# Kernel tuning notes

Measured on AMD Instinct MI355X. Metric: run time of the kernel, lower is better.

## Reference

```python
import jax, jax.numpy as jnp
import numpy as np
import math

EPS = 1e-12  # F.normalize default eps

def _l2_normalize(x):
    n = jnp.sqrt(jnp.sum(x * x, axis=-1, keepdims=True))
    return x / jnp.maximum(n, EPS)

def setup_inputs() -> dict:
    key = jax.random.key(0)
    k1, k2 = jax.random.split(key)
    B, F, C = 16384, 1024, 1000
    features = jax.random.normal(k1, (B, F), dtype=jnp.float32)
    prototypes = jax.random.normal(k2, (C, F), dtype=jnp.float32)
    distance_scale = jnp.ones((1,), dtype=jnp.float32)
    temperature = jnp.ones((1,), dtype=jnp.float32)
    return {"features": features, "prototypes": prototypes,
            "distance_scale": distance_scale, "temperature": temperature}

def reference(features, prototypes, distance_scale, temperature):
    # L2-normalize both sides (F.normalize, p=2, eps=1e-12)
    f = _l2_normalize(features)      # [B, F]
    p = _l2_normalize(prototypes)    # [C, F]
    # Pairwise Euclidean distance. For unit vectors ||f-p||^2 = 2 - 2 f.p,
    # clamped at 0 for numerical safety; then / sqrt(2).
    sim = jnp.einsum('bf,cf->bc', f, p)                  # [B, C]
    sq = jnp.maximum(2.0 - 2.0 * sim, 0.0)
    distances = jnp.sqrt(sq) / jnp.float32(math.sqrt(2.0))
    iso = jnp.abs(distance_scale) * distances            # [B, C]
    logits = -(iso + jnp.mean(iso, axis=1, keepdims=True))
    return logits / temperature
```

## Files before the change

### kernel.cpp

```cpp
#include <hip/hip_runtime.h>
#include <hip/hip_bf16.h>
#include <math.h>

#define B_ROWS 16384
#define C_COLS 1000
#define C_PAD  1024
#define FDIM   1024
#define FBLKS  4096
#define FP8_SCALE 256.0f
#define INV_SIM   (1.0f / (FP8_SCALE * FP8_SCALE))

typedef __attribute__((ext_vector_type(8))) short bf16x8;
typedef __attribute__((ext_vector_type(4))) float f32x4;
typedef __attribute__((ext_vector_type(4))) int   i32x4;
typedef __attribute__((ext_vector_type(8))) int   i32x8;

#define GLD_LDS(gp, lp) __builtin_amdgcn_global_load_lds( \
    (__attribute__((address_space(1))) void*)(gp),        \
    (__attribute__((address_space(3))) void*)(lp), 16, 0, 0)

__global__ __launch_bounds__(256) void normalize_all(
    const float* __restrict__ feat, const float* __restrict__ prot,
    unsigned char* __restrict__ fb, unsigned char* __restrict__ pb,
    float* __restrict__ rowsum)
{
    const int lane = threadIdx.x & 63;
    const int wave = threadIdx.x >> 6;

    if (blockIdx.x < 64) rowsum[blockIdx.x * 256 + threadIdx.x] = 0.0f;

    const float* in;
    unsigned char* out;
    int row, nvalid;
    if (blockIdx.x < FBLKS) {
        row = blockIdx.x * 4 + wave;  in = feat; out = fb; nvalid = B_ROWS;
    } else {
        row = (blockIdx.x - FBLKS) * 4 + wave;  in = prot; out = pb; nvalid = C_COLS;
    }
    unsigned char* orow = out + (size_t)row * FDIM;

    if (row >= nvalid) {
        i32x4 z = {0, 0, 0, 0};
        ((i32x4*)orow)[lane] = z;
        return;
    }

    const float4* rp = (const float4*)(in + (size_t)row * FDIM);
    float4 v[4];
    float ss = 0.0f;
    #pragma unroll
    for (int c = 0; c < 4; ++c) {
        v[c] = rp[lane * 4 + c];
        ss += v[c].x * v[c].x + v[c].y * v[c].y + v[c].z * v[c].z + v[c].w * v[c].w;
    }
    #pragma unroll
    for (int off = 1; off < 64; off <<= 1) ss += __shfl_xor(ss, off, 64);
    const float inv = FP8_SCALE / sqrtf(fmaxf(ss, 1e-24f));

    i32x4 pk;
    #pragma unroll
    for (int c = 0; c < 4; ++c) {
        int w0 = __builtin_amdgcn_cvt_pk_fp8_f32(v[c].x * inv, v[c].y * inv, 0, false);
        w0     = __builtin_amdgcn_cvt_pk_fp8_f32(v[c].z * inv, v[c].w * inv, w0, true);
        pk[c] = w0;
    }
    ((i32x4*)orow)[lane] = pk;
}

__global__ __launch_bounds__(256) void gemm_dist(
    const unsigned char* __restrict__ A,
    const unsigned char* __restrict__ Bp,
    __hip_bfloat16* __restrict__ D,
    float* __restrict__ rowsum)
{
    __shared__ unsigned char As[128 * 128];
    __shared__ unsigned char Bs[128 * 128];

    const int tid  = threadIdx.x;
    const int lane = tid & 63;
    const int wave = tid >> 6;

    const int id  = blockIdx.x;
    const int xcd = id & 7;
    const int seq = id >> 3;
    const int bn  = seq & 7;
    const int bm  = xcd * 16 + (seq >> 3);

    const int waveM = (wave >> 1) * 64;
    const int waveN = (wave & 1) * 64;

    f32x4 acc[4][4] = {};

    const int srow8 = lane >> 3;
    const int sg    = (lane & 7) ^ srow8;
    const unsigned char* Abase = A  + ((size_t)(bm * 128 + wave * 8 + srow8)) * FDIM + sg * 16;
    const unsigned char* Bbase = Bp + ((size_t)(bn * 128 + wave * 8 + srow8)) * FDIM + sg * 16;

    const int q2   = (lane >> 4) * 2;
    const int bxor = lane & 7;
    const int fA = (waveM + (lane & 15)) * 128;
    const int fB = (waveN + (lane & 15)) * 128;
    const int pg0 = ((q2)     ^ bxor) * 16;
    const int pg1 = ((q2 + 1) ^ bxor) * 16;

    #pragma unroll 1
    for (int k0 = 0; k0 < FDIM; k0 += 128) {
        __syncthreads();
        #pragma unroll
        for (int r = 0; r < 4; ++r) {
            GLD_LDS(Abase + (size_t)(r * 32) * FDIM + k0, &As[(r * 32 + wave * 8) * 128]);
            GLD_LDS(Bbase + (size_t)(r * 32) * FDIM + k0, &Bs[(r * 32 + wave * 8) * 128]);
        }
        __syncthreads();

        i32x8 b[4];
        #pragma unroll
        for (int nt = 0; nt < 4; ++nt) {
            const i32x4 lo = *(const i32x4*)&Bs[fB + nt * 2048 + pg0];
            const i32x4 hi = *(const i32x4*)&Bs[fB + nt * 2048 + pg1];
            b[nt] = (i32x8){lo.x, lo.y, lo.z, lo.w, hi.x, hi.y, hi.z, hi.w};
        }
        #pragma unroll
        for (int mt = 0; mt < 4; ++mt) {
            const i32x4 lo = *(const i32x4*)&As[fA + mt * 2048 + pg0];
            const i32x4 hi = *(const i32x4*)&As[fA + mt * 2048 + pg1];
            const i32x8 a = (i32x8){lo.x, lo.y, lo.z, lo.w, hi.x, hi.y, hi.z, hi.w};
            #pragma unroll
            for (int nt = 0; nt < 4; ++nt)
                acc[mt][nt] = __builtin_amdgcn_mfma_scale_f32_16x16x128_f8f6f4(
                    a, b[nt], acc[mt][nt], 0, 0, 0, 127, 0, 127);
        }
    }

    const int row0 = bm * 128 + waveM;
    const int col0 = bn * 128 + waveN;
    #pragma unroll
    for (int mt = 0; mt < 4; ++mt) {
        #pragma unroll
        for (int r = 0; r < 4; ++r) {
            const int row = row0 + mt * 16 + (lane >> 4) * 4 + r;
            float part = 0.0f;
            #pragma unroll
            for (int nt = 0; nt < 4; ++nt) {
                const int col = col0 + nt * 16 + (lane & 15);
                const float sim = acc[mt][nt][r] * INV_SIM;
                const float dv = sqrtf(fmaxf(1.0f - sim, 0.0f));
                if (col < C_COLS) {
                    D[(size_t)row * C_COLS + col] = __float2bfloat16(dv);
                    part += dv;
                }
            }
            part += __shfl_xor(part, 1, 64);
            part += __shfl_xor(part, 2, 64);
            part += __shfl_xor(part, 4, 64);
            part += __shfl_xor(part, 8, 64);
            if ((lane & 15) == 0) atomicAdd(&rowsum[row], part);
        }
    }
}

__global__ __launch_bounds__(256) void finalize(
    const __hip_bfloat16* __restrict__ D, const float* __restrict__ rowsum,
    const float* __restrict__ scale, const float* __restrict__ temp,
    float* __restrict__ out)
{
    const size_t i = (size_t)blockIdx.x * 256 + threadIdx.x;
    const float a = -fabsf(scale[0]) / temp[0];
    const int row = (int)((i * 8) / C_COLS);
    const float m = rowsum[row] * (1.0f / (float)C_COLS);

    const bf16x8 dv = *(const bf16x8*)(D + i * 8);
    const __hip_bfloat16* dp = (const __hip_bfloat16*)&dv;
    float4 o0, o1;
    o0.x = a * (__bfloat162float(dp[0]) + m);
    o0.y = a * (__bfloat162float(dp[1]) + m);
    o0.z = a * (__bfloat162float(dp[2]) + m);
    o0.w = a * (__bfloat162float(dp[3]) + m);
    o1.x = a * (__bfloat162float(dp[4]) + m);
    o1.y = a * (__bfloat162float(dp[5]) + m);
    o1.z = a * (__bfloat162float(dp[6]) + m);
    o1.w = a * (__bfloat162float(dp[7]) + m);
    ((float4*)out)[i * 2]     = o0;
    ((float4*)out)[i * 2 + 1] = o1;
}

extern "C" void kernel_launch(void* const* d_in, const int* in_sizes, int n_in,
                              void* d_out, int out_size, void* d_ws, size_t ws_size,
                              hipStream_t stream)
{
    const float* features = (const float*)d_in[0];
    const float* protos   = (const float*)d_in[1];
    const float* dscale   = (const float*)d_in[2];
    const float* temp     = (const float*)d_in[3];
    float* out = (float*)d_out;

    char* ws = (char*)d_ws;
    unsigned char* fb = (unsigned char*)ws;
    unsigned char* pb = (unsigned char*)(ws + 16777216);
    __hip_bfloat16* D = (__hip_bfloat16*)(ws + 17825792);
    float* rowsum     = (float*)(ws + 50593792);

    normalize_all<<<FBLKS + C_PAD / 4, 256, 0, stream>>>(features, protos, fb, pb, rowsum);

    gemm_dist<<<1024, 256, 0, stream>>>(fb, pb, D, rowsum);

    finalize<<<(B_ROWS * C_COLS / 8) / 256, 256, 0, stream>>>(D, rowsum, dscale, temp, out);
}
```

Baseline: 159.3 us.

## Fuse distance GEMM and finalize via cooperative grid sync, keeping distances in registers

Adds a cooperative-launch kernel that computes the FP8 GEMM and distance values, accumulates per-row sums atomically, then waits on a grid-wide barrier. After the barrier it reads the completed row means and writes the final fp32 logits directly from registers. This removes the bf16 intermediate distance buffer (write and re-read of about 32 MB) and the separate finalize launch. In exchange, all 1024 blocks must be co-resident (launch bounds 256,4), which may limit registers, and the grid barrier adds sync cost. If cooperative launch is unavailable it falls back to the old two-kernel path.

```diff
diff --git a/kernel.cpp b/kernel.cpp
--- a/kernel.cpp
+++ b/kernel.cpp
@@ -1,4 +1,5 @@
 #include <hip/hip_runtime.h>
+#include <hip/hip_cooperative_groups.h>
 #include <hip/hip_bf16.h>
 #include <math.h>
 
@@ -65,6 +66,117 @@
         pk[c] = w0;
     }
     ((i32x4*)orow)[lane] = pk;
+}
+
+__global__ __launch_bounds__(256, 4) void gemm_dist_out(
+    const unsigned char* __restrict__ A,
+    const unsigned char* __restrict__ Bp,
+    float* __restrict__ rowsum,
+    const float* __restrict__ scale,
+    const float* __restrict__ temp,
+    float* __restrict__ out)
+{
+    __shared__ unsigned char As[128 * 128];
+    __shared__ unsigned char Bs[128 * 128];
+
+    const int tid  = threadIdx.x;
+    const int lane = tid & 63;
+    const int wave = tid >> 6;
+
+    const int id  = blockIdx.x;
+    const int xcd = id & 7;
+    const int seq = id >> 3;
+    const int bn  = seq & 7;
+    const int bm  = xcd * 16 + (seq >> 3);
+
+    const int waveM = (wave >> 1) * 64;
+    const int waveN = (wave & 1) * 64;
+
+    f32x4 acc[4][4] = {};
+
+    const int srow8 = lane >> 3;
+    const int sg    = (lane & 7) ^ srow8;
+    const unsigned char* Abase = A  + ((size_t)(bm * 128 + wave * 8 + srow8)) * FDIM + sg * 16;
+    const unsigned char* Bbase = Bp + ((size_t)(bn * 128 + wave * 8 + srow8)) * FDIM + sg * 16;
+
+    const int q2   = (lane >> 4) * 2;
+    const int bxor = lane & 7;
+    const int fA = (waveM + (lane & 15)) * 128;
+    const int fB = (waveN + (lane & 15)) * 128;
+    const int pg0 = ((q2)     ^ bxor) * 16;
+    const int pg1 = ((q2 + 1) ^ bxor) * 16;
+
+    #pragma unroll 1
+    for (int k0 = 0; k0 < FDIM; k0 += 128) {
+        __syncthreads();
+        #pragma unroll
+        for (int r = 0; r < 4; ++r) {
+            GLD_LDS(Abase + (size_t)(r * 32) * FDIM + k0, &As[(r * 32 + wave * 8) * 128]);
+            GLD_LDS(Bbase + (size_t)(r * 32) * FDIM + k0, &Bs[(r * 32 + wave * 8) * 128]);
+        }
+        __syncthreads();
+
+        i32x8 b[4];
+        #pragma unroll
+        for (int nt = 0; nt < 4; ++nt) {
+            const i32x4 lo = *(const i32x4*)&Bs[fB + nt * 2048 + pg0];
+            const i32x4 hi = *(const i32x4*)&Bs[fB + nt * 2048 + pg1];
+            b[nt] = (i32x8){lo.x, lo.y, lo.z, lo.w, hi.x, hi.y, hi.z, hi.w};
+        }
+        #pragma unroll
+        for (int mt = 0; mt < 4; ++mt) {
+            const i32x4 lo = *(const i32x4*)&As[fA + mt * 2048 + pg0];
+            const i32x4 hi = *(const i32x4*)&As[fA + mt * 2048 + pg1];
+            const i32x8 a = (i32x8){lo.x, lo.y, lo.z, lo.w, hi.x, hi.y, hi.z, hi.w};
+            #pragma unroll
+            for (int nt = 0; nt < 4; ++nt)
+                acc[mt][nt] = __builtin_amdgcn_mfma_scale_f32_16x16x128_f8f6f4(
+                    a, b[nt], acc[mt][nt], 0, 0, 0, 127, 0, 127);
+        }
+    }
+
+    const int row0 = bm * 128 + waveM;
+    const int col0 = bn * 128 + waveN;
+    #pragma unroll
+    for (int mt = 0; mt < 4; ++mt) {
+        #pragma unroll
+        for (int r = 0; r < 4; ++r) {
+            float part = 0.0f;
+            #pragma unroll
+            for (int nt = 0; nt < 4; ++nt) {
+                const float sim = acc[mt][nt][r] * INV_SIM;
+                const float dv = sqrtf(fmaxf(1.0f - sim, 0.0f));
+                acc[mt][nt][r] = dv;
+                const int col = col0 + nt * 16 + (lane & 15);
+                if (col < C_COLS) part += dv;
+            }
+            part += __shfl_xor(part, 1, 64);
+            part += __shfl_xor(part, 2, 64);
+            part += __shfl_xor(part, 4, 64);
+            part += __shfl_xor(part, 8, 64);
+            if ((lane & 15) == 0)
+                atomicAdd(&rowsum[row0 + mt * 16 + (lane >> 4) * 4 + r], part);
+        }
+    }
+
+    cooperative_groups::this_grid().sync();
+
+    const float aS = -fabsf(scale[0]) / temp[0];
+    #pragma unroll
+    for (int mt = 0; mt < 4; ++mt) {
+        #pragma unroll
+        for (int r = 0; r < 4; ++r) {
+            const int row = row0 + mt * 16 + (lane >> 4) * 4 + r;
+            const float m = __hip_atomic_load(&rowsum[row], __ATOMIC_RELAXED,
+                                              __HIP_MEMORY_SCOPE_AGENT) * (1.0f / (float)C_COLS);
+            #pragma unroll
+            for (int nt = 0; nt < 4; ++nt) {
+                const int col = col0 + nt * 16 + (lane & 15);
+                if (col < C_COLS)
+                    out[(size_t)row * C_COLS + col] = aS * (acc[mt][nt][r] + m);
+            }
+        }
+    }
 }
 
 __global__ __launch_bounds__(256) void gemm_dist(
@@ -202,7 +314,37 @@
 
     normalize_all<<<FBLKS + C_PAD / 4, 256, 0, stream>>>(features, protos, fb, pb, rowsum);
 
-    gemm_dist<<<1024, 256, 0, stream>>>(fb, pb, D, rowsum);
-
-    finalize<<<(B_ROWS * C_COLS / 8) / 256, 256, 0, stream>>>(D, rowsum, dscale, temp, out);
-}
+    static int use_coop = -1;
+    if (use_coop < 0) {
+        int dev = 0;
+        (void)hipGetDevice(&dev);
+        int coopOK = 0;
+        (void)hipDeviceGetAttribute(&coopOK, hipDeviceAttributeCooperativeLaunch, dev);
+        int numCU = 0;
+        (void)hipDeviceGetAttribute(&numCU, hipDeviceAttributeMultiprocessorCount, dev);
+        int maxB = 0;
+        hipError_t oe = hipOccupancyMaxActiveBlocksPerMultiprocessor(
+            &maxB, reinterpret_cast<const void*>(gemm_dist_out), 256, 0);
+        use_coop = (coopOK && oe == hipSuccess && numCU > 0 &&
+                    (long)maxB * numCU >= 1024) ? 1 : 0;
+    }
+
+    if (use_coop) {
+        const unsigned char* gA = fb;
+        const unsigned char* gB = pb;
+        float* gR = rowsum;
+        const float* gS = dscale;
+        const float* gT = temp;
+        float* gO = out;
+        void* kargs[] = { (void*)&gA, (void*)&gB, (void*)&gR,
+                          (void*)&gS, (void*)&gT, (void*)&gO };
+        hipError_t le = hipLaunchCooperativeKernel(
+            reinterpret_cast<const void*>(gemm_dist_out),
+            dim3(1024), dim3(256), kargs, 0, stream);
+        if (le != hipSuccess) use_coop = 0;
+    }
+    if (!use_coop) {
+        gemm_dist<<<1024, 256, 0, stream>>>(fb, pb, D, rowsum);
+        finalize<<<(B_ROWS * C_COLS / 8) / 256, 256, 0, stream>>>(D, rowsum, dscale, temp, out);
+    }
+}
```

New measurement: 160.7 us. No clear change (+0.9%).

## Enlarge GEMM tile to 256x256 with double-buffered LDS prefetch pipeline

Applied to the files above, without the earlier changes.

The fp8 GEMM kernel grows its block tile from 128x128 to 256x256 and uses 8 waves of 512 threads, each wave computing 128x64. It double-buffers the K tiles in 128KB of dynamic LDS, prefetching two stages ahead with explicit vmcnt waits, and raises wave priority around the MFMA bursts. The aim is to raise data reuse per LDS byte and hide global-to-LDS load latency behind compute. In exchange it launches only 256 blocks, which may underfill the 256 CUs, and it carries higher register pressure from 32 accumulators per wave.

```diff
diff --git a/kernel.cpp b/kernel.cpp
--- a/kernel.cpp
+++ b/kernel.cpp
@@ -67,14 +67,15 @@
     ((i32x4*)orow)[lane] = pk;
 }
 
-__global__ __launch_bounds__(256) void gemm_dist(
+__global__ __launch_bounds__(512, 2) void gemm_dist(
     const unsigned char* __restrict__ A,
     const unsigned char* __restrict__ Bp,
     __hip_bfloat16* __restrict__ D,
     float* __restrict__ rowsum)
 {
-    __shared__ unsigned char As[128 * 128];
-    __shared__ unsigned char Bs[128 * 128];
+    extern __shared__ unsigned char LDS[];
+    unsigned char* As = LDS;
+    unsigned char* Bs = LDS + 65536;
 
     const int tid  = threadIdx.x;
     const int lane = tid & 63;
@@ -83,18 +84,19 @@
     const int id  = blockIdx.x;
     const int xcd = id & 7;
     const int seq = id >> 3;
-    const int bn  = seq & 7;
-    const int bm  = xcd * 16 + (seq >> 3);
-
-    const int waveM = (wave >> 1) * 64;
-    const int waveN = (wave & 1) * 64;
-
-    f32x4 acc[4][4] = {};
+    const int bn  = seq & 3;
+    const int bm  = xcd * 8 + (seq >> 2);
+
+    const int waveM = (wave >> 2) * 128;
+    const int waveN = (wave & 3) * 64;
+
+    f32x4 acc[8][4] = {};
 
     const int srow8 = lane >> 3;
     const int sg    = (lane & 7) ^ srow8;
-    const unsigned char* Abase = A  + ((size_t)(bm * 128 + wave * 8 + srow8)) * FDIM + sg * 16;
-    const unsigned char* Bbase = Bp + ((size_t)(bn * 128 + wave * 8 + srow8)) * FDIM + sg * 16;
+    const unsigned char* Abase = A  + ((size_t)(bm * 256 + wave * 32 + srow8)) * FDIM + sg * 16;
+    const unsigned char* Bbase = Bp + ((size_t)(bn * 256 + wave * 32 + srow8)) * FDIM + sg * 16;
+    const int ldsW = wave * 4096;
 
     const int q2   = (lane >> 4) * 2;
     const int bxor = lane & 7;
@@ -103,39 +105,84 @@
     const int pg0 = ((q2)     ^ bxor) * 16;
     const int pg1 = ((q2 + 1) ^ bxor) * 16;
 
+#define STAGE_BATCH(K0_, BUF_) do {                                                  \
+        _Pragma("unroll")                                                            \
+        for (int r_ = 0; r_ < 4; ++r_)                                               \
+            GLD_LDS(Abase + (size_t)(r_ * 8) * FDIM + (K0_), &As[(BUF_) + ldsW + r_ * 1024]); \
+        _Pragma("unroll")                                                            \
+        for (int r_ = 0; r_ < 4; ++r_)                                               \
+            GLD_LDS(Bbase + (size_t)(r_ * 8) * FDIM + (K0_), &Bs[(BUF_) + ldsW + r_ * 1024]); \
+    } while (0)
+
+#define COMPUTE_STEP(CUR_) do {                                                      \
+        i32x8 b4[4], a4[4];                                                          \
+        _Pragma("unroll")                                                            \
+        for (int nt = 0; nt < 4; ++nt) {                                             \
+            ((i32x4*)&b4[nt])[0] = *(const i32x4*)&Bs[(CUR_) + fB + nt * 2048 + pg0];\
+            ((i32x4*)&b4[nt])[1] = *(const i32x4*)&Bs[(CUR_) + fB + nt * 2048 + pg1];\
+        }                                                                            \
+        _Pragma("unroll")                                                            \
+        for (int mt = 0; mt < 4; ++mt) {                                             \
+            ((i32x4*)&a4[mt])[0] = *(const i32x4*)&As[(CUR_) + fA + mt * 2048 + pg0];\
+            ((i32x4*)&a4[mt])[1] = *(const i32x4*)&As[(CUR_) + fA + mt * 2048 + pg1];\
+        }                                                                            \
+        __builtin_amdgcn_s_setprio(1);                                               \
+        _Pragma("unroll")                                                            \
+        for (int mt = 0; mt < 4; ++mt)                                               \
+            _Pragma("unroll")                                                        \
+            for (int nt = 0; nt < 4; ++nt)                                           \
+                acc[mt][nt] = __builtin_amdgcn_mfma_scale_f32_16x16x128_f8f6f4(      \
+                    a4[mt], b4[nt], acc[mt][nt], 0, 0, 0, 127, 0, 127);              \
+        __builtin_amdgcn_s_setprio(0);                                               \
+        _Pragma("unroll")                                                            \
+        for (int mt = 0; mt < 4; ++mt) {                                             \
+            ((i32x4*)&a4[mt])[0] = *(const i32x4*)&As[(CUR_) + fA + (mt + 4) * 2048 + pg0]; \
+            ((i32x4*)&a4[mt])[1] = *(const i32x4*)&As[(CUR_) + fA + (mt + 4) * 2048 + pg1]; \
+        }                                                                            \
+        __builtin_amdgcn_s_setprio(1);                                               \
+        _Pragma("unroll")                                                            \
+        for (int mt = 0; mt < 4; ++mt)                                               \
+            _Pragma("unroll")                                                        \
+            for (int nt = 0; nt < 4; ++nt)                                           \
+                acc[mt + 4][nt] = __builtin_amdgcn_mfma_scale_f32_16x16x128_f8f6f4(  \
+                    a4[mt], b4[nt], acc[mt + 4][nt], 0, 0, 0, 127, 0, 127);          \
+        __builtin_amdgcn_s_setprio(0);                                               \
+    } while (0)
+
+    STAGE_BATCH(0, 0);
+    __builtin_amdgcn_sched_barrier(0);
+    STAGE_BATCH(128, 32768);
+    __builtin_amdgcn_sched_barrier(0);
+
     #pragma unroll 1
-    for (int k0 = 0; k0 < FDIM; k0 += 128) {
-        __syncthreads();
-        #pragma unroll
-        for (int r = 0; r < 4; ++r) {
-            GLD_LDS(Abase + (size_t)(r * 32) * FDIM + k0, &As[(r * 32 + wave * 8) * 128]);
-            GLD_LDS(Bbase + (size_t)(r * 32) * FDIM + k0, &Bs[(r * 32 + wave * 8) * 128]);
+    for (int t = 0; t < 7; ++t) {
+        asm volatile("s_waitcnt vmcnt(8)" ::: "memory");
+        __builtin_amdgcn_s_barrier();
+        __builtin_amdgcn_sched_barrier(0);
+
+        const int cur = (t & 1) << 15;
+
+        COMPUTE_STEP(cur);
+
+        asm volatile("s_waitcnt lgkmcnt(0)" ::: "memory");
+        __builtin_amdgcn_s_barrier();
+        __builtin_amdgcn_sched_barrier(0);
+        if (t < 6) {
+            const int k0n = (t + 2) * 128;
+            STAGE_BATCH(k0n, cur);
+            __builtin_amdgcn_sched_barrier(0);
         }
-        __syncthreads();
-
-        i32x8 b[4];
-        #pragma unroll
-        for (int nt = 0; nt < 4; ++nt) {
-            const i32x4 lo = *(const i32x4*)&Bs[fB + nt * 2048 + pg0];
-            const i32x4 hi = *(const i32x4*)&Bs[fB + nt * 2048 + pg1];
-            b[nt] = (i32x8){lo.x, lo.y, lo.z, lo.w, hi.x, hi.y, hi.z, hi.w};
-        }
-        #pragma unroll
-        for (int mt = 0; mt < 4; ++mt) {
-            const i32x4 lo = *(const i32x4*)&As[fA + mt * 2048 + pg0];
-            const i32x4 hi = *(const i32x4*)&As[fA + mt * 2048 + pg1];
-            const i32x8 a = (i32x8){lo.x, lo.y, lo.z, lo.w, hi.x, hi.y, hi.z, hi.w};
-            #pragma unroll
-            for (int nt = 0; nt < 4; ++nt)
-                acc[mt][nt] = __builtin_amdgcn_mfma_scale_f32_16x16x128_f8f6f4(
-                    a, b[nt], acc[mt][nt], 0, 0, 0, 127, 0, 127);
-        }
-    }
-
-    const int row0 = bm * 128 + waveM;
-    const int col0 = bn * 128 + waveN;
-    #pragma unroll
-    for (int mt = 0; mt < 4; ++mt) {
+    }
+
+    asm volatile("s_waitcnt vmcnt(0)" ::: "memory");
+    __builtin_amdgcn_s_barrier();
+    __builtin_amdgcn_sched_barrier(0);
+    COMPUTE_STEP(32768);
+
+    const int row0 = bm * 256 + waveM;
+    const int col0 = bn * 256 + waveN;
+    #pragma unroll
+    for (int mt = 0; mt < 8; ++mt) {
         #pragma unroll
         for (int r = 0; r < 4; ++r) {
             const int row = row0 + mt * 16 + (lane >> 4) * 4 + r;
@@ -200,9 +247,16 @@
     __hip_bfloat16* D = (__hip_bfloat16*)(ws + 17825792);
     float* rowsum     = (float*)(ws + 50593792);
 
+    static int lds_ok = 0;
+    if (!lds_ok) {
+        (void)hipFuncSetAttribute(reinterpret_cast<const void*>(gemm_dist),
+                                  hipFuncAttributeMaxDynamicSharedMemorySize, 131072);
+        lds_ok = 1;
+    }
+
     normalize_all<<<FBLKS + C_PAD / 4, 256, 0, stream>>>(features, protos, fb, pb, rowsum);
 
-    gemm_dist<<<1024, 256, 0, stream>>>(fb, pb, D, rowsum);
+    gemm_dist<<<256, 512, 131072, stream>>>(fb, pb, D, rowsum);
 
     finalize<<<(B_ROWS * C_COLS / 8) / 256, 256, 0, stream>>>(D, rowsum, dscale, temp, out);
 }
```

Result: no change. 159.9 us (+0.4%).
